# Performance work log

Hardware: AMD Instinct MI355X
Metric: run time of the kernel (lower is better)

Reference implementation:

```python
import jax, jax.numpy as jnp
import numpy as np

B, S, HID = 1, 2048, 2048
HQ, HKV, D = 16, 4, 128
BS = 64            # seerattn gate block size
GH = 128           # gate hidden size
INTER = 5632
THR = 0.004        # seerattn_threshold on softmaxed block gate scores
EPS = 1e-6
NEG = -1e30


def _rms(x, w):
    xf = x.astype(jnp.float32)
    var = jnp.mean(xf * xf, axis=-1, keepdims=True)
    return (w * (xf * jax.lax.rsqrt(var + EPS))).astype(x.dtype)


def _rotate_half(x):
    x1, x2 = jnp.split(x, 2, axis=-1)
    return jnp.concatenate([-x2, x1], axis=-1)


def setup_inputs() -> dict:
    key = jax.random.key(0)
    ks = jax.random.split(key, 16)
    s = 0.02
    pos = jnp.arange(S, dtype=jnp.float32)
    inv_freq = 1.0 / (1e6 ** (jnp.arange(0, D, 2, dtype=jnp.float32) / D))
    freqs = pos[:, None] * inv_freq[None, :]
    emb = jnp.concatenate([freqs, freqs], axis=-1)  # [S, D]
    return {
        'hidden_states': jax.random.normal(ks[0], (B, S, HID), jnp.float32),
        'cos': jnp.cos(emb),
        'sin': jnp.sin(emb),
        'ln1_w': jnp.ones((HID,), jnp.float32),
        'ln2_w': jnp.ones((HID,), jnp.float32),
        'Wq': jax.random.normal(ks[1], (HID, HQ * D), jnp.float32) * s,
        'bq': jnp.zeros((HQ * D,), jnp.float32),
        'Wk': jax.random.normal(ks[2], (HID, HKV * D), jnp.float32) * s,
        'bk': jnp.zeros((HKV * D,), jnp.float32),
        'Wv': jax.random.normal(ks[3], (HID, HKV * D), jnp.float32) * s,
        'bv': jnp.zeros((HKV * D,), jnp.float32),
        'Wo': jax.random.normal(ks[4], (HQ * D, HID), jnp.float32) * s,
        'gWq': jax.random.normal(ks[5], (D, GH), jnp.float32) * s,
        'gWk': jax.random.normal(ks[6], (D, GH), jnp.float32) * s,
        'Wgate': jax.random.normal(ks[7], (HID, INTER), jnp.float32) * s,
        'Wup': jax.random.normal(ks[8], (HID, INTER), jnp.float32) * s,
        'Wdown': jax.random.normal(ks[9], (INTER, HID), jnp.float32) * s,
    }


def reference(hidden_states, cos, sin, ln1_w, ln2_w, Wq, bq, Wk, bk, Wv, bv, Wo,
              gWq, gWk, Wgate, Wup, Wdown):
    B_, S_, _ = hidden_states.shape
    QB = S_ // BS
    grp = HQ // HKV

    h = _rms(hidden_states, ln1_w)
    q = (h @ Wq + bq).reshape(B_, S_, HQ, D)
    k = (h @ Wk + bk).reshape(B_, S_, HKV, D)
    v = (h @ Wv + bv).reshape(B_, S_, HKV, D)

    # ---- learned block gate (pre-RoPE q/k), threshold sparsity method ----
    qg = jnp.einsum('bshd,dg->bshg', q, gWq)
    qg = qg.reshape(B_, QB, BS, HQ, GH).mean(axis=2)            # [B, QB, HQ, GH]
    kp = k.reshape(B_, QB, BS, HKV, D).mean(axis=2)             # block-pooled K
    kg = jnp.einsum('bkhd,dg->bkhg', kp, gWk)
    kg = jnp.repeat(kg, grp, axis=2)                            # GQA -> HQ heads
    gscore = jnp.einsum('bqhg,bkhg->bhqk', qg, kg) * (GH ** -0.5)

    bidx = jnp.arange(QB)
    blk_causal = bidx[:, None] >= bidx[None, :]                 # [QB, QB]
    gscore = jnp.where(blk_causal[None, None], gscore, NEG)
    gate = jax.nn.softmax(gscore, axis=-1)                      # [B, HQ, QB, QB]

    diag = bidx[:, None] == bidx[None, :]
    keep = blk_causal[None, None] & ((gate >= THR) | diag[None, None])

    # ---- RoPE (unsqueeze_dim=2, layout [B,S,H,D]) ----
    c = cos[None, :, None, :]
    sn = sin[None, :, None, :]
    q = q * c + _rotate_half(q) * sn
    k = k * c + _rotate_half(k) * sn

    k = jnp.repeat(k, grp, axis=2)
    v = jnp.repeat(v, grp, axis=2)

    # ---- block-sparse masked attention (reference: dense w/ block mask) ----
    scores = jnp.einsum('bqhd,bkhd->bhqk', q, k) * (D ** -0.5)
    tok_keep = jnp.repeat(jnp.repeat(keep, BS, axis=2), BS, axis=3)
    tidx = jnp.arange(S_)
    tok_causal = tidx[:, None] >= tidx[None, :]
    mask = tok_keep & tok_causal[None, None]
    scores = jnp.where(mask, scores, NEG)
    p = jax.nn.softmax(scores, axis=-1)
    o = jnp.einsum('bhqk,bkhd->bqhd', p, v).reshape(B_, S_, HQ * D)
    attn_out = o @ Wo

    h2 = hidden_states + attn_out
    h3 = _rms(h2, ln2_w)
    mlp = (jax.nn.silu(h3 @ Wgate) * (h3 @ Wup)) @ Wdown
    return h2 + mlp
```

## Files before the change

### kernel.cpp

```cpp
#include <hip/hip_runtime.h>
#include <stdint.h>
#include <stddef.h>

#define S_LEN 2048
#define HIDN  2048
#define HQ    16
#define HKV   4
#define HDIM  128
#define NQKV  3072
#define QBLK  32
#define GHW   128
#define INTER 5632
#define NEGF  (-1e30f)
#define THRG  0.004f

typedef short bf16x8 __attribute__((ext_vector_type(8)));
typedef float f32x4  __attribute__((ext_vector_type(4)));

__device__ __forceinline__ short f2bf(float f) {
  union { float f; unsigned u; } v; v.f = f;
  unsigned r = (v.u + 0x7FFFu + ((v.u >> 16) & 1u)) >> 16;
  return (short)r;
}
__device__ __forceinline__ float bf2f(short s) {
  union { float f; unsigned u; } v; v.u = ((unsigned)(unsigned short)s) << 16;
  return v.f;
}
__device__ __forceinline__ void gload16(const void* g, void* l) {
  __builtin_amdgcn_global_load_lds(
      (const __attribute__((address_space(1))) void*)g,
      (__attribute__((address_space(3))) void*)l, 16, 0, 0);
}
__device__ __forceinline__ unsigned pack_bf2(float hi, float lo) {
  return __builtin_amdgcn_perm(__float_as_uint(hi), __float_as_uint(lo), 0x07060302u);
}

__global__ __launch_bounds__(256) void k_transpose_cast(
    const float* __restrict__ src, short* __restrict__ dst, int R, int C) {
  __shared__ float t[32][33];
  const int tx = threadIdx.x, ty = threadIdx.y;
  const int x = blockIdx.x * 32 + tx;
  const int y0 = blockIdx.y * 32;
#pragma unroll
  for (int i = 0; i < 4; i++) {
    int yy = ty + i * 8;
    t[yy][tx] = src[(long)(y0 + yy) * C + x];
  }
  __syncthreads();
  const int xo = blockIdx.y * 32 + tx;
  const int yo0 = blockIdx.x * 32;
#pragma unroll
  for (int i = 0; i < 4; i++) {
    int yy = ty + i * 8;
    dst[(long)(yo0 + yy) * R + xo] = f2bf(t[tx][yy]);
  }
}

__global__ void k_bias_concat(const float* __restrict__ bq, const float* __restrict__ bk,
                              const float* __restrict__ bv, float* __restrict__ out) {
  int i = blockIdx.x * 256 + threadIdx.x;
  if (i < 2048) out[i] = bq[i];
  else if (i < 2560) out[i] = bk[i - 2048];
  else out[i] = bv[i - 2560];
}

__global__ __launch_bounds__(256) void k_rms(const float* __restrict__ x,
                                             const float* __restrict__ w,
                                             short* __restrict__ out) {
  const int row = blockIdx.x;
  const float* xr = x + (long)row * HIDN;
  float v[8];
  float ss = 0.f;
#pragma unroll
  for (int i = 0; i < 8; i++) {
    v[i] = xr[threadIdx.x + i * 256];
    ss += v[i] * v[i];
  }
#pragma unroll
  for (int off = 32; off > 0; off >>= 1) ss += __shfl_down(ss, off, 64);
  __shared__ float red[4];
  const int wave = threadIdx.x >> 6, lane = threadIdx.x & 63;
  if (lane == 0) red[wave] = ss;
  __syncthreads();
  float tot = red[0] + red[1] + red[2] + red[3];
  float rs = rsqrtf(tot / (float)HIDN + 1e-6f);
#pragma unroll
  for (int i = 0; i < 8; i++) {
    int c = threadIdx.x + i * 256;
    out[(long)row * HIDN + c] = f2bf(v[i] * rs * w[c]);
  }
}

__global__ __launch_bounds__(256) void k_rms_fin(const float* __restrict__ p0,
                                                 const float* __restrict__ hid,
                                                 const float* __restrict__ w,
                                                 float* __restrict__ h2,
                                                 short* __restrict__ out) {
  const int row = blockIdx.x;
  const long base = (long)row * HIDN;
  float v[8];
  float ss = 0.f;
#pragma unroll
  for (int i = 0; i < 8; i++) {
    int c = threadIdx.x + i * 256;
    float t = p0[base + c] + h2[base + c] + hid[base + c];
    h2[base + c] = t;
    v[i] = t;
    ss += t * t;
  }
#pragma unroll
  for (int off = 32; off > 0; off >>= 1) ss += __shfl_down(ss, off, 64);
  __shared__ float red[4];
  const int wave = threadIdx.x >> 6, lane = threadIdx.x & 63;
  if (lane == 0) red[wave] = ss;
  __syncthreads();
  float tot = red[0] + red[1] + red[2] + red[3];
  float rs = rsqrtf(tot / (float)HIDN + 1e-6f);
#pragma unroll
  for (int i = 0; i < 8; i++) {
    int c = threadIdx.x + i * 256;
    out[base + c] = f2bf(v[i] * rs * w[c]);
  }
}

template <int MODE, int BN>
__global__ __launch_bounds__(256) void k_gemm(
    const short* __restrict__ A, const short* __restrict__ Bt,
    float* __restrict__ Cf, float* __restrict__ Cf2,
    short* __restrict__ Cb, short* __restrict__ Cb2,
    const float* __restrict__ bias, const float* __restrict__ add,
    int M, int N, int K, int ksl) {
  constexpr int NT = BN / 32;
  constexpr int BIW = BN / 32;
  constexpr int BPP = BN / 16;
  __shared__ short As[2][128][32];
  __shared__ short Bs[2][BN][32];
  const int tid = threadIdx.x;
  const int wave = tid >> 6, lane = tid & 63, quad = lane >> 4, l15 = lane & 15;
  const long m0 = (long)blockIdx.y * 128, n0 = (long)blockIdx.x * BN;
  const int wr = (wave >> 1) * 64, wc = (wave & 1) * (BN / 2);
  const int i2 = lane >> 2, i3 = lane & 3;
  f32x4 acc[4][NT] = {};
  const short* Ainst[4];
  short* Alds[4];
#pragma unroll
  for (int j = 0; j < 4; j++) {
    const int g = wave * 4 + j, h = g >> 3, rb = (g & 7) * 16;
    Ainst[j] = A + (m0 + rb + i2) * K + h * 32 + i3 * 8;
    Alds[j] = &As[h][rb][0];
  }
  const short* Binst[BIW];
  short* Blds[BIW];
#pragma unroll
  for (int j = 0; j < BIW; j++) {
    const int g = wave * BIW + j, h = g / BPP, rb = (g % BPP) * 16;
    Binst[j] = Bt + (n0 + rb + i2) * K + h * 32 + i3 * 8;
    Blds[j] = &Bs[h][rb][0];
  }
  const int kbeg = (MODE == 4) ? blockIdx.z * ksl : 0;
  const int kend = kbeg + ((MODE == 4) ? ksl : K);
  for (int k0 = kbeg; k0 < kend; k0 += 64) {
    __syncthreads();
#pragma unroll
    for (int j = 0; j < 4; j++) gload16(Ainst[j] + k0, Alds[j]);
#pragma unroll
    for (int j = 0; j < BIW; j++) gload16(Binst[j] + k0, Blds[j]);
    __syncthreads();
#pragma unroll
    for (int s = 0; s < 2; s++) {
      bf16x8 af[4], bb[NT];
#pragma unroll
      for (int mi = 0; mi < 4; mi++)
        af[mi] = *(const bf16x8*)&As[s][wr + mi * 16 + l15][quad * 8];
#pragma unroll
      for (int ni = 0; ni < NT; ni++)
        bb[ni] = *(const bf16x8*)&Bs[s][wc + ni * 16 + l15][quad * 8];
#pragma unroll
      for (int mi = 0; mi < 4; mi++)
#pragma unroll
        for (int ni = 0; ni < NT; ni++)
          acc[mi][ni] = __builtin_amdgcn_mfma_f32_16x16x32_bf16(af[mi], bb[ni], acc[mi][ni], 0, 0, 0);
    }
  }
  const bool hb = (MODE == 0) && (bias != nullptr);
  const bool ha = (MODE == 0) && (add != nullptr);
  float* dstp = (MODE == 4) ? ((blockIdx.z == 0) ? Cf : Cf2) : Cf;
#pragma unroll
  for (int mi = 0; mi < 4; mi++) {
#pragma unroll
    for (int ni = 0; ni < NT; ni++) {
      long mbase = m0 + wr + mi * 16 + quad * 4;
      long n = n0 + wc + ni * 16 + l15;
#pragma unroll
      for (int r = 0; r < 4; r++) {
        float v = acc[mi][ni][r];
        if (MODE == 0) {
          long idx = (mbase + r) * N + n;
          if (hb) v += bias[n];
          if (ha) v += add[idx];
          Cf[idx] = v;
        } else if (MODE == 3) {
          short* db = Cb;
          long nn = n;
          if (nn >= INTER) { db = Cb2; nn -= INTER; }
          db[(mbase + r) * INTER + nn] = f2bf(v);
        } else {
          dstp[(mbase + r) * N + n] = v;
        }
      }
    }
  }
}

__global__ __launch_bounds__(256) void k_silu(const short* __restrict__ u,
                                              short* __restrict__ g) {
  const long n = (long)S_LEN * INTER;
  for (long i = ((long)blockIdx.x * 256 + threadIdx.x) * 8; i < n;
       i += (long)gridDim.x * 256 * 8) {
    bf16x8 gv = *(const bf16x8*)(g + i);
    bf16x8 uv = *(const bf16x8*)(u + i);
    bf16x8 o;
#pragma unroll
    for (int j = 0; j < 8; j++) {
      float gf = bf2f(gv[j]);
      float uf = bf2f(uv[j]);
      float sg = gf / (1.f + __expf(-gf));
      o[j] = f2bf(sg * uf);
    }
    *(bf16x8*)(g + i) = o;
  }
}

__global__ __launch_bounds__(256) void k_finish(const float* __restrict__ p0,
                                                const float* __restrict__ h2,
                                                float* __restrict__ out) {
  const long n = (long)S_LEN * HIDN;
  for (long i = ((long)blockIdx.x * 256 + threadIdx.x) * 4; i < n;
       i += (long)gridDim.x * 256 * 4) {
    float4 a = *(const float4*)(out + i);
    float4 b = *(const float4*)(p0 + i);
    float4 c = *(const float4*)(h2 + i);
    a.x += b.x + c.x;
    a.y += b.y + c.y;
    a.z += b.z + c.z;
    a.w += b.w + c.w;
    *(float4*)(out + i) = a;
  }
}

__global__ __launch_bounds__(256) void k_blockmean(const float* __restrict__ qkv,
                                                   float* __restrict__ qm,
                                                   float* __restrict__ km) {
  int id = blockIdx.x * 256 + threadIdx.x;
  int qb = id / 2560, c = id % 2560;
  const float* base = qkv + (long)qb * 64 * NQKV + c;
  float acc = 0.f;
  for (int s = 0; s < 64; s++) acc += base[(long)s * NQKV];
  acc *= (1.f / 64.f);
  if (c < 2048) qm[(long)qb * 2048 + c] = acc;
  else km[(long)qb * 512 + (c - 2048)] = acc;
}

__global__ __launch_bounds__(128) void k_gateproj(const float* __restrict__ qm,
                                                  const float* __restrict__ km,
                                                  const float* __restrict__ gWq,
                                                  const float* __restrict__ gWk,
                                                  float* __restrict__ qg,
                                                  float* __restrict__ kg) {
  __shared__ float xm[128];
  const int b = blockIdx.x;
  const float* src; const float* W; float* dst;
  if (b < 512) { src = qm + (long)b * 128; W = gWq; dst = qg + (long)b * 128; }
  else { int r = b - 512; src = km + (long)r * 128; W = gWk; dst = kg + (long)r * 128; }
  xm[threadIdx.x] = src[threadIdx.x];
  __syncthreads();
  float acc = 0.f;
  for (int d = 0; d < 128; d++) acc += xm[d] * W[d * GHW + threadIdx.x];
  dst[threadIdx.x] = acc;
}

__global__ __launch_bounds__(64) void k_gatemask(const float* __restrict__ qg,
                                                 const float* __restrict__ kg,
                                                 unsigned char* __restrict__ mask) {
  const int qb = blockIdx.x, h = blockIdx.y;
  __shared__ float qv[128];
  const int t = threadIdx.x;
  qv[t] = qg[((long)qb * 16 + h) * 128 + t];
  qv[t + 64] = qg[((long)qb * 16 + h) * 128 + t + 64];
  __syncthreads();
  const int kb = t;
  float s = NEGF;
  if (kb < 32 && kb <= qb) {
    const float* kr = kg + ((long)kb * 4 + (h >> 2)) * 128;
    float acc = 0.f;
    for (int d = 0; d < 128; d++) acc += qv[d] * kr[d];
    s = acc * 0.08838834764831845f;
  }
  float m = s;
#pragma unroll
  for (int off = 32; off > 0; off >>= 1) m = fmaxf(m, __shfl_xor(m, off, 64));
  float e = (kb < 32 && kb <= qb) ? __expf(s - m) : 0.f;
  float sum = e;
#pragma unroll
  for (int off = 32; off > 0; off >>= 1) sum += __shfl_xor(sum, off, 64);
  if (kb < 32) {
    float gate = e / sum;
    bool keep = (kb <= qb) && (gate >= THRG || kb == qb);
    mask[((long)h * 32 + qb) * 32 + kb] = keep ? 1 : 0;
  }
}

__global__ __launch_bounds__(256) void k_rope(const float* __restrict__ qkv,
                                              const float* __restrict__ cosb,
                                              const float* __restrict__ sinb,
                                              short* __restrict__ q_bf,
                                              short* __restrict__ k_bf) {
  long id = (long)blockIdx.x * 256 + threadIdx.x;
  int d = (int)(id & 63);
  long rest = id >> 6;
  int head = (int)(rest % 20);
  int s = (int)(rest / 20);
  const float c = cosb[(long)s * HDIM + d];
  const float sn = sinb[(long)s * HDIM + d];
  if (head < HQ) {
    const float* src = qkv + (long)s * NQKV + head * HDIM;
    float x1 = src[d], x2 = src[d + 64];
    short* dst = q_bf + ((long)head * S_LEN + s) * HDIM;
    dst[d] = f2bf(x1 * c - x2 * sn);
    dst[d + 64] = f2bf(x2 * c + x1 * sn);
  } else {
    int hk = head - HQ;
    const float* src = qkv + (long)s * NQKV + 2048 + hk * HDIM;
    float x1 = src[d], x2 = src[d + 64];
    short* dst = k_bf + ((long)hk * S_LEN + s) * HDIM;
    dst[d] = f2bf(x1 * c - x2 * sn);
    dst[d + 64] = f2bf(x2 * c + x1 * sn);
  }
}

__global__ __launch_bounds__(256) void k_vcast_t(const float* __restrict__ qkv,
                                                 short* __restrict__ v_t) {
  __shared__ float t[32][33];
  const int hk = blockIdx.z;
  const int tx = threadIdx.x, ty = threadIdx.y;
  const int d0 = blockIdx.x * 32;
  const int s0 = blockIdx.y * 32;
  const float* src = qkv + 2560 + (long)hk * HDIM;
#pragma unroll
  for (int i = 0; i < 4; i++) {
    int s = ty + i * 8;
    t[s][tx] = src[(long)(s0 + s) * NQKV + d0 + tx];
  }
  __syncthreads();
  short* dst = v_t + (long)hk * HDIM * S_LEN;
#pragma unroll
  for (int i = 0; i < 4; i++) {
    int d = ty + i * 8;
    dst[(long)(d0 + d) * S_LEN + s0 + tx] = f2bf(t[tx][d]);
  }
}

__global__ __launch_bounds__(256) void k_attn(const short* __restrict__ q_bf,
                                              const short* __restrict__ k_bf,
                                              const short* __restrict__ v_t,
                                              const unsigned char* __restrict__ mask,
                                              short* __restrict__ o_bf) {
  const int qb = blockIdx.x, h = blockIdx.y;
  const int tid = threadIdx.x, wave = tid >> 6, lane = tid & 63;
  const int quad = lane >> 4, l15 = lane & 15;
  __shared__ short Ks[4 * 64 * 32];
  __shared__ short Vs[2 * 128 * 32];
  __shared__ short Ps[4][16 * 72];
  short* Pw = Ps[wave];
  const int hk = h >> 2;
  const unsigned char* mptr = mask + ((long)h * 32 + qb) * 32;
  const float SCL = 0.08838834764831845f * 1.4426950408889634f;
  const int qrow_g = qb * 64 + wave * 16 + l15;

  bf16x8 bq[4];
  {
    const short* qrp = q_bf + ((long)h * S_LEN + qrow_g) * HDIM + quad * 8;
#pragma unroll
    for (int kd = 0; kd < 4; kd++) bq[kd] = *(const bf16x8*)(qrp + kd * 32);
  }

  const short* kh = k_bf + (long)hk * S_LEN * HDIM;
  const short* vh = v_t + (long)hk * HDIM * S_LEN;

  const int i2 = lane >> 2, i3 = lane & 3;
  int koff[4], voff[4];
  const int vp = wave >> 1, vhh = wave & 1;
#pragma unroll
  for (int inst = 0; inst < 4; inst++) {
    koff[inst] = (inst * 16 + i2) * HDIM + wave * 32 + i3 * 8;
    voff[inst] = (vhh * 64 + inst * 16 + i2) * S_LEN + vp * 32 + i3 * 8;
  }

  f32x4 accO[8] = {};
  float mrow = -3.0e38f, lrow = 0.f;

  for (int kb = 0; kb <= qb; kb++) {
    if (!mptr[kb]) continue;
    __syncthreads();
    {
      const int kg = kb * 64 * HDIM;
      const int vg = kb * 64;
#pragma unroll
      for (int inst = 0; inst < 4; inst++) {
        gload16(kh + kg + koff[inst], &Ks[wave * 2048 + inst * 512]);
        gload16(vh + vg + voff[inst], &Vs[vp * 4096 + (vhh * 64 + inst * 16) * 32]);
      }
    }
    __syncthreads();

    f32x4 sv[4];
#pragma unroll
    for (int nt = 0; nt < 4; nt++) {
      f32x4 t = {};
#pragma unroll
      for (int kd = 0; kd < 4; kd++) {
        bf16x8 ka = *(const bf16x8*)&Ks[kd * 2048 + (nt * 16 + l15) * 32 + quad * 8];
        t = __builtin_amdgcn_mfma_f32_16x16x32_bf16(ka, bq[kd], t, 0, 0, 0);
      }
      sv[nt] = t;
    }
    float lmx = -__builtin_inff();
    if (kb < qb) {
#pragma unroll
      for (int nt = 0; nt < 4; nt++)
#pragma unroll
        for (int r = 0; r < 4; r++) {
          sv[nt][r] *= SCL;
          lmx = fmaxf(lmx, sv[nt][r]);
        }
    } else {
#pragma unroll
      for (int nt = 0; nt < 4; nt++)
#pragma unroll
        for (int r = 0; r < 4; r++) {
          const int kcol = kb * 64 + nt * 16 + quad * 4 + r;
          sv[nt][r] = (kcol <= qrow_g) ? sv[nt][r] * SCL : -__builtin_inff();
          lmx = fmaxf(lmx, sv[nt][r]);
        }
    }
    lmx = fmaxf(lmx, __shfl_xor(lmx, 16, 64));
    lmx = fmaxf(lmx, __shfl_xor(lmx, 32, 64));
    const float mnew = fmaxf(mrow, lmx);
    const float alpha = __builtin_amdgcn_exp2f(mrow - mnew);
    mrow = mnew;
    float psum = 0.f;
#pragma unroll
    for (int nt = 0; nt < 4; nt++) {
#pragma unroll
      for (int r = 0; r < 4; r++) {
        float p = __builtin_amdgcn_exp2f(sv[nt][r] - mnew);
        sv[nt][r] = p;
        psum += p;
      }
      uint2 u;
      u.x = pack_bf2(sv[nt][1], sv[nt][0]);
      u.y = pack_bf2(sv[nt][3], sv[nt][2]);
      *(uint2*)&Pw[l15 * 72 + nt * 16 + quad * 4] = u;
    }
    psum += __shfl_xor(psum, 16, 64);
    psum += __shfl_xor(psum, 32, 64);
    lrow = lrow * alpha + psum;
    float al[4];
#pragma unroll
    for (int r = 0; r < 4; r++) al[r] = __shfl(alpha, quad * 4 + r, 64);
#pragma unroll
    for (int dt = 0; dt < 8; dt++)
#pragma unroll
      for (int r = 0; r < 4; r++) accO[dt][r] *= al[r];
    asm volatile("s_waitcnt lgkmcnt(0)" ::: "memory");
    bf16x8 pf[2];
#pragma unroll
    for (int ksb = 0; ksb < 2; ksb++)
      pf[ksb] = *(const bf16x8*)&Pw[l15 * 72 + ksb * 32 + quad * 8];
#pragma unroll
    for (int dt = 0; dt < 8; dt++) {
#pragma unroll
      for (int ksb = 0; ksb < 2; ksb++) {
        bf16x8 vf = *(const bf16x8*)&Vs[ksb * 4096 + (dt * 16 + l15) * 32 + quad * 8];
        accO[dt] = __builtin_amdgcn_mfma_f32_16x16x32_bf16(pf[ksb], vf, accO[dt], 0, 0, 0);
      }
    }
  }
  const float linv = 1.f / lrow;
  float li[4];
#pragma unroll
  for (int r = 0; r < 4; r++) li[r] = __shfl(linv, quad * 4 + r, 64);
#pragma unroll
  for (int r = 0; r < 4; r++) {
    const long srow = (long)qb * 64 + wave * 16 + quad * 4 + r;
#pragma unroll
    for (int dt = 0; dt < 8; dt++)
      o_bf[srow * HIDN + h * HDIM + dt * 16 + l15] = f2bf(accO[dt][r] * li[r]);
  }
}

static constexpr size_t SZ_WQKVT = (size_t)NQKV * HIDN * 2;
static constexpr size_t SZ_WOT = (size_t)HIDN * HIDN * 2;
static constexpr size_t SZ_WBIG = (size_t)INTER * HIDN * 2;
static constexpr size_t OFF_WQKVT = 0;
static constexpr size_t OFF_WOT = OFF_WQKVT + SZ_WQKVT;
static constexpr size_t OFF_WGATET = OFF_WOT + SZ_WOT;
static constexpr size_t OFF_WUPT = OFF_WGATET + SZ_WBIG;
static constexpr size_t OFF_WDOWNT = OFF_WUPT + SZ_WBIG;
static constexpr size_t OFF_BIAS = OFF_WDOWNT + SZ_WBIG;
static constexpr size_t OFF_MASK = OFF_BIAS + 3072 * 4 + 4096;
static constexpr size_t OFF_QM = OFF_MASK + 16 * 32 * 32 + 4096;
static constexpr size_t OFF_KM = OFF_QM + (size_t)32 * 16 * 128 * 4;
static constexpr size_t OFF_QG = OFF_KM + (size_t)32 * 4 * 128 * 4;
static constexpr size_t OFF_KG = OFF_QG + (size_t)32 * 16 * 128 * 4;
static constexpr size_t OFF_H2 = OFF_KG + (size_t)32 * 4 * 128 * 4;
static constexpr size_t OFF_H3 = OFF_H2 + (size_t)S_LEN * HIDN * 4;
static constexpr size_t OFF_REGA = OFF_H3 + (size_t)S_LEN * HIDN * 2;
static constexpr size_t RA_HBF = 0;
static constexpr size_t RA_QBF = RA_HBF + (size_t)S_LEN * HIDN * 2;
static constexpr size_t RA_KBF = RA_QBF + (size_t)HQ * S_LEN * HDIM * 2;
static constexpr size_t RA_VT = RA_KBF + (size_t)HKV * S_LEN * HDIM * 2;
static constexpr size_t RA_OBF = RA_VT + (size_t)HKV * HDIM * S_LEN * 2;
static constexpr size_t SZ_REGA = RA_OBF + (size_t)S_LEN * HIDN * 2;
static constexpr size_t OFF_REGB = OFF_REGA + SZ_REGA;
static constexpr size_t SZ_REGB = (size_t)S_LEN * NQKV * 4;
static constexpr size_t TOTAL_WS = OFF_REGB + SZ_REGB;

extern "C" void kernel_launch(void* const* d_in, const int* in_sizes, int n_in,
                              void* d_out, int out_size, void* d_ws, size_t ws_size,
                              hipStream_t stream) {
  const float* hidden = (const float*)d_in[0];
  const float* cosb = (const float*)d_in[1];
  const float* sinb = (const float*)d_in[2];
  const float* ln1 = (const float*)d_in[3];
  const float* ln2 = (const float*)d_in[4];
  const float* Wq = (const float*)d_in[5];
  const float* bq = (const float*)d_in[6];
  const float* Wk = (const float*)d_in[7];
  const float* bk = (const float*)d_in[8];
  const float* Wv = (const float*)d_in[9];
  const float* bv = (const float*)d_in[10];
  const float* Wo = (const float*)d_in[11];
  const float* gWq = (const float*)d_in[12];
  const float* gWk = (const float*)d_in[13];
  const float* Wgate = (const float*)d_in[14];
  const float* Wup = (const float*)d_in[15];
  const float* Wdown = (const float*)d_in[16];

  if (ws_size < TOTAL_WS) return;

  char* ws = (char*)d_ws;
  short* WqkvT = (short*)(ws + OFF_WQKVT);
  short* WoT = (short*)(ws + OFF_WOT);
  short* WgateT = (short*)(ws + OFF_WGATET);
  short* WupT = (short*)(ws + OFF_WUPT);
  short* WdownT = (short*)(ws + OFF_WDOWNT);
  float* biasqkv = (float*)(ws + OFF_BIAS);
  unsigned char* maskb = (unsigned char*)(ws + OFF_MASK);
  float* qm = (float*)(ws + OFF_QM);
  float* km = (float*)(ws + OFF_KM);
  float* qg = (float*)(ws + OFF_QG);
  float* kg = (float*)(ws + OFF_KG);
  float* h2 = (float*)(ws + OFF_H2);
  short* h3_bf = (short*)(ws + OFF_H3);
  short* h_bf = (short*)(ws + OFF_REGA + RA_HBF);
  short* q_bf = (short*)(ws + OFF_REGA + RA_QBF);
  short* k_bf = (short*)(ws + OFF_REGA + RA_KBF);
  short* v_t = (short*)(ws + OFF_REGA + RA_VT);
  short* o_bf = (short*)(ws + OFF_REGA + RA_OBF);
  short* u_bf = (short*)(ws + OFF_REGA);
  float* p0b = (float*)(ws + OFF_REGA);
  float* qkv_f = (float*)(ws + OFF_REGB);
  float* p0a = (float*)(ws + OFF_REGB);
  short* g_bf = (short*)(ws + OFF_REGB);
  float* outp = (float*)d_out;

  dim3 tb(32, 8);
  k_transpose_cast<<<dim3(64, 64), tb, 0, stream>>>(Wq, WqkvT, HIDN, 2048);
  k_transpose_cast<<<dim3(16, 64), tb, 0, stream>>>(Wk, WqkvT + (size_t)2048 * HIDN, HIDN, 512);
  k_transpose_cast<<<dim3(16, 64), tb, 0, stream>>>(Wv, WqkvT + (size_t)2560 * HIDN, HIDN, 512);
  k_transpose_cast<<<dim3(64, 64), tb, 0, stream>>>(Wo, WoT, HIDN, HIDN);
  k_transpose_cast<<<dim3(176, 64), tb, 0, stream>>>(Wgate, WgateT, HIDN, INTER);
  k_transpose_cast<<<dim3(176, 64), tb, 0, stream>>>(Wup, WupT, HIDN, INTER);
  k_transpose_cast<<<dim3(64, 176), tb, 0, stream>>>(Wdown, WdownT, INTER, HIDN);
  k_bias_concat<<<12, 256, 0, stream>>>(bq, bk, bv, biasqkv);

  k_rms<<<S_LEN, 256, 0, stream>>>(hidden, ln1, h_bf);
  k_gemm<0, 64><<<dim3(NQKV / 64, S_LEN / 128), 256, 0, stream>>>(
      h_bf, WqkvT, qkv_f, nullptr, nullptr, nullptr, biasqkv, nullptr, S_LEN, NQKV, HIDN, HIDN);
  k_blockmean<<<320, 256, 0, stream>>>(qkv_f, qm, km);
  k_gateproj<<<640, 128, 0, stream>>>(qm, km, gWq, gWk, qg, kg);
  k_gatemask<<<dim3(32, 16), 64, 0, stream>>>(qg, kg, maskb);
  k_rope<<<10240, 256, 0, stream>>>(qkv_f, cosb, sinb, q_bf, k_bf);
  k_vcast_t<<<dim3(4, 64, 4), tb, 0, stream>>>(qkv_f, v_t);
  k_attn<<<dim3(32, 16), 256, 0, stream>>>(q_bf, k_bf, v_t, maskb, o_bf);
  k_gemm<4, 64><<<dim3(HIDN / 64, S_LEN / 128, 2), 256, 0, stream>>>(
      o_bf, WoT, p0a, h2, nullptr, nullptr, nullptr, nullptr, S_LEN, HIDN, HIDN, HIDN / 2);
  k_rms_fin<<<S_LEN, 256, 0, stream>>>(p0a, hidden, ln2, h2, h3_bf);
  k_gemm<3, 128><<<dim3(2 * INTER / 128, S_LEN / 128), 256, 0, stream>>>(
      h3_bf, WgateT, nullptr, nullptr, g_bf, u_bf, nullptr, nullptr, S_LEN, 2 * INTER, HIDN, HIDN);
  k_silu<<<2048, 256, 0, stream>>>(u_bf, g_bf);
  k_gemm<4, 64><<<dim3(HIDN / 64, S_LEN / 128, 2), 256, 0, stream>>>(
      g_bf, WdownT, p0b, outp, nullptr, nullptr, nullptr, nullptr, S_LEN, HIDN, INTER, INTER / 2);
  k_finish<<<2048, 256, 0, stream>>>(p0b, h2, outp);
  (void)in_sizes; (void)n_in; (void)out_size;
}
```

Measured before the change: 636.7 us.

## Interleave gate/up weight rows and fuse SiLU-multiply into GEMM epilogue

Transposes Wgate and Wup into one weight matrix whose rows alternate in 16-row groups. Each gate 16-column tile then sits next to its matching up tile inside a wave's accumulators. The GEMM gets a new epilogue mode that computes silu(g)*u directly and writes a single bf16 activation. This removes the separate SiLU kernel and the bf16 round trip of both gate and up outputs. It relies on the interleave lining up with the per-wave tile column layout (NT even, wc offsets).

```diff
diff --git a/kernel.cpp b/kernel.cpp
--- a/kernel.cpp
+++ b/kernel.cpp
@@ -56,6 +56,28 @@
   }
 }
 
+__global__ __launch_bounds__(256) void k_transpose_cast_ilv(
+    const float* __restrict__ src, short* __restrict__ dst, int R, int C, int phase) {
+  __shared__ float t[32][33];
+  const int tx = threadIdx.x, ty = threadIdx.y;
+  const int x = blockIdx.x * 32 + tx;
+  const int y0 = blockIdx.y * 32;
+#pragma unroll
+  for (int i = 0; i < 4; i++) {
+    int yy = ty + i * 8;
+    t[yy][tx] = src[(long)(y0 + yy) * C + x];
+  }
+  __syncthreads();
+  const int xo = blockIdx.y * 32 + tx;
+  const int yo0 = blockIdx.x * 32;
+#pragma unroll
+  for (int i = 0; i < 4; i++) {
+    int j = yo0 + ty + i * 8;
+    long orow = (long)(j >> 4) * 32 + phase * 16 + (j & 15);
+    dst[orow * R + xo] = f2bf(t[tx][ty + i * 8]);
+  }
+}
+
 __global__ void k_bias_concat(const float* __restrict__ bq, const float* __restrict__ bk,
                               const float* __restrict__ bv, float* __restrict__ out) {
   int i = blockIdx.x * 256 + threadIdx.x;
@@ -127,7 +149,7 @@
 __global__ __launch_bounds__(256) void k_gemm(
     const short* __restrict__ A, const short* __restrict__ Bt,
     float* __restrict__ Cf, float* __restrict__ Cf2,
-    short* __restrict__ Cb, short* __restrict__ Cb2,
+    short* __restrict__ Cb,
     const float* __restrict__ bias, const float* __restrict__ add,
     int M, int N, int K, int ksl) {
   constexpr int NT = BN / 32;
@@ -187,47 +209,38 @@
   float* dstp = (MODE == 4) ? ((blockIdx.z == 0) ? Cf : Cf2) : Cf;
 #pragma unroll
   for (int mi = 0; mi < 4; mi++) {
-#pragma unroll
-    for (int ni = 0; ni < NT; ni++) {
-      long mbase = m0 + wr + mi * 16 + quad * 4;
-      long n = n0 + wc + ni * 16 + l15;
-#pragma unroll
-      for (int r = 0; r < 4; r++) {
-        float v = acc[mi][ni][r];
-        if (MODE == 0) {
-          long idx = (mbase + r) * N + n;
-          if (hb) v += bias[n];
-          if (ha) v += add[idx];
-          Cf[idx] = v;
-        } else if (MODE == 3) {
-          short* db = Cb;
-          long nn = n;
-          if (nn >= INTER) { db = Cb2; nn -= INTER; }
-          db[(mbase + r) * INTER + nn] = f2bf(v);
-        } else {
-          dstp[(mbase + r) * N + n] = v;
+    if (MODE == 5) {
+#pragma unroll
+      for (int ni2 = 0; ni2 < NT / 2; ni2++) {
+        long mbase = m0 + wr + mi * 16 + quad * 4;
+        long col = (n0 + wc) / 2 + ni2 * 16 + l15;
+#pragma unroll
+        for (int r = 0; r < 4; r++) {
+          float g = acc[mi][2 * ni2][r];
+          float u = acc[mi][2 * ni2 + 1][r];
+          float sg = g / (1.f + __expf(-g));
+          Cb[(mbase + r) * INTER + col] = f2bf(sg * u);
+        }
+      }
+    } else {
+#pragma unroll
+      for (int ni = 0; ni < NT; ni++) {
+        long mbase = m0 + wr + mi * 16 + quad * 4;
+        long n = n0 + wc + ni * 16 + l15;
+#pragma unroll
+        for (int r = 0; r < 4; r++) {
+          float v = acc[mi][ni][r];
+          if (MODE == 0) {
+            long idx = (mbase + r) * N + n;
+            if (hb) v += bias[n];
+            if (ha) v += add[idx];
+            Cf[idx] = v;
+          } else {
+            dstp[(mbase + r) * N + n] = v;
+          }
         }
       }
     }
-  }
-}
-
-__global__ __launch_bounds__(256) void k_silu(const short* __restrict__ u,
-                                              short* __restrict__ g) {
-  const long n = (long)S_LEN * INTER;
-  for (long i = ((long)blockIdx.x * 256 + threadIdx.x) * 8; i < n;
-       i += (long)gridDim.x * 256 * 8) {
-    bf16x8 gv = *(const bf16x8*)(g + i);
-    bf16x8 uv = *(const bf16x8*)(u + i);
-    bf16x8 o;
-#pragma unroll
-    for (int j = 0; j < 8; j++) {
-      float gf = bf2f(gv[j]);
-      float uf = bf2f(uv[j]);
-      float sg = gf / (1.f + __expf(-gf));
-      o[j] = f2bf(sg * uf);
-    }
-    *(bf16x8*)(g + i) = o;
   }
 }
 
@@ -504,9 +517,8 @@
 static constexpr size_t SZ_WBIG = (size_t)INTER * HIDN * 2;
 static constexpr size_t OFF_WQKVT = 0;
 static constexpr size_t OFF_WOT = OFF_WQKVT + SZ_WQKVT;
-static constexpr size_t OFF_WGATET = OFF_WOT + SZ_WOT;
-static constexpr size_t OFF_WUPT = OFF_WGATET + SZ_WBIG;
-static constexpr size_t OFF_WDOWNT = OFF_WUPT + SZ_WBIG;
+static constexpr size_t OFF_WGU = OFF_WOT + SZ_WOT;
+static constexpr size_t OFF_WDOWNT = OFF_WGU + 2 * SZ_WBIG;
 static constexpr size_t OFF_BIAS = OFF_WDOWNT + SZ_WBIG;
 static constexpr size_t OFF_MASK = OFF_BIAS + 3072 * 4 + 4096;
 static constexpr size_t OFF_QM = OFF_MASK + 16 * 32 * 32 + 4096;
@@ -552,8 +564,7 @@
   char* ws = (char*)d_ws;
   short* WqkvT = (short*)(ws + OFF_WQKVT);
   short* WoT = (short*)(ws + OFF_WOT);
-  short* WgateT = (short*)(ws + OFF_WGATET);
-  short* WupT = (short*)(ws + OFF_WUPT);
+  short* Wgu = (short*)(ws + OFF_WGU);
   short* WdownT = (short*)(ws + OFF_WDOWNT);
   float* biasqkv = (float*)(ws + OFF_BIAS);
   unsigned char* maskb = (unsigned char*)(ws + OFF_MASK);
@@ -568,11 +579,10 @@
   short* k_bf = (short*)(ws + OFF_REGA + RA_KBF);
   short* v_t = (short*)(ws + OFF_REGA + RA_VT);
   short* o_bf = (short*)(ws + OFF_REGA + RA_OBF);
-  short* u_bf = (short*)(ws + OFF_REGA);
   float* p0b = (float*)(ws + OFF_REGA);
   float* qkv_f = (float*)(ws + OFF_REGB);
   float* p0a = (float*)(ws + OFF_REGB);
-  short* g_bf = (short*)(ws + OFF_REGB);
+  short* act_bf = (short*)(ws + OFF_REGB);
   float* outp = (float*)d_out;
 
   dim3 tb(32, 8);
@@ -580,14 +590,14 @@
   k_transpose_cast<<<dim3(16, 64), tb, 0, stream>>>(Wk, WqkvT + (size_t)2048 * HIDN, HIDN, 512);
   k_transpose_cast<<<dim3(16, 64), tb, 0, stream>>>(Wv, WqkvT + (size_t)2560 * HIDN, HIDN, 512);
   k_transpose_cast<<<dim3(64, 64), tb, 0, stream>>>(Wo, WoT, HIDN, HIDN);
-  k_transpose_cast<<<dim3(176, 64), tb, 0, stream>>>(Wgate, WgateT, HIDN, INTER);
-  k_transpose_cast<<<dim3(176, 64), tb, 0, stream>>>(Wup, WupT, HIDN, INTER);
+  k_transpose_cast_ilv<<<dim3(176, 64), tb, 0, stream>>>(Wgate, Wgu, HIDN, INTER, 0);
+  k_transpose_cast_ilv<<<dim3(176, 64), tb, 0, stream>>>(Wup, Wgu, HIDN, INTER, 1);
   k_transpose_cast<<<dim3(64, 176), tb, 0, stream>>>(Wdown, WdownT, INTER, HIDN);
   k_bias_concat<<<12, 256, 0, stream>>>(bq, bk, bv, biasqkv);
 
   k_rms<<<S_LEN, 256, 0, stream>>>(hidden, ln1, h_bf);
   k_gemm<0, 64><<<dim3(NQKV / 64, S_LEN / 128), 256, 0, stream>>>(
-      h_bf, WqkvT, qkv_f, nullptr, nullptr, nullptr, biasqkv, nullptr, S_LEN, NQKV, HIDN, HIDN);
+      h_bf, WqkvT, qkv_f, nullptr, nullptr, biasqkv, nullptr, S_LEN, NQKV, HIDN, HIDN);
   k_blockmean<<<320, 256, 0, stream>>>(qkv_f, qm, km);
   k_gateproj<<<640, 128, 0, stream>>>(qm, km, gWq, gWk, qg, kg);
   k_gatemask<<<dim3(32, 16), 64, 0, stream>>>(qg, kg, maskb);
@@ -595,13 +605,12 @@
   k_vcast_t<<<dim3(4, 64, 4), tb, 0, stream>>>(qkv_f, v_t);
   k_attn<<<dim3(32, 16), 256, 0, stream>>>(q_bf, k_bf, v_t, maskb, o_bf);
   k_gemm<4, 64><<<dim3(HIDN / 64, S_LEN / 128, 2), 256, 0, stream>>>(
-      o_bf, WoT, p0a, h2, nullptr, nullptr, nullptr, nullptr, S_LEN, HIDN, HIDN, HIDN / 2);
+      o_bf, WoT, p0a, h2, nullptr, nullptr, nullptr, S_LEN, HIDN, HIDN, HIDN / 2);
   k_rms_fin<<<S_LEN, 256, 0, stream>>>(p0a, hidden, ln2, h2, h3_bf);
-  k_gemm<3, 128><<<dim3(2 * INTER / 128, S_LEN / 128), 256, 0, stream>>>(
-      h3_bf, WgateT, nullptr, nullptr, g_bf, u_bf, nullptr, nullptr, S_LEN, 2 * INTER, HIDN, HIDN);
-  k_silu<<<2048, 256, 0, stream>>>(u_bf, g_bf);
+  k_gemm<5, 128><<<dim3(2 * INTER / 128, S_LEN / 128), 256, 0, stream>>>(
+      h3_bf, Wgu, nullptr, nullptr, act_bf, nullptr, nullptr, S_LEN, 2 * INTER, HIDN, HIDN);
   k_gemm<4, 64><<<dim3(HIDN / 64, S_LEN / 128, 2), 256, 0, stream>>>(
-      g_bf, WdownT, p0b, outp, nullptr, nullptr, nullptr, nullptr, S_LEN, HIDN, INTER, INTER / 2);
+      act_bf, WdownT, p0b, outp, nullptr, nullptr, nullptr, S_LEN, HIDN, INTER, INTER / 2);
   k_finish<<<2048, 256, 0, stream>>>(p0b, h2, outp);
   (void)in_sizes; (void)n_in; (void)out_size;
 }
```

Result: faster. 620.6 us (-2.5%).
